# Kernel tuning notes

Hardware: AMD Instinct MI355X
Metric: run time of the kernel (lower is better)

The kernel has to match this reference:

```python
import jax, jax.numpy as jnp
import numpy as np

B, C, H, W = 8, 256, 64, 64
NH, FF, L, K = 8, 1024, 3, 64
THR = 0.5
DH = C // NH
SCALE = 1.0 / float(np.sqrt(DH))
N = H * W


def setup_inputs() -> dict:
    key = jax.random.key(0)
    ks = jax.random.split(key, 16)
    s = 0.02
    rn = lambda k, shape: (jax.random.normal(k, shape, jnp.float32) * s)
    return {
        "x": jax.random.normal(ks[0], (B, C, H, W), jnp.float32),
        "y": jax.random.normal(ks[1], (B, C, H, W), jnp.float32),
        "proj_w": rn(ks[2], (C, 2 * C)), "proj_b": rn(ks[3], (C,)),
        "sal_w": rn(ks[4], (1, C)), "sal_b": rn(ks[5], (1,)),
        "soft_w": rn(ks[6], (2, K, C)), "soft_b": rn(ks[7], (2, K)),
        "attn_in_w": rn(ks[8], (2, L, 3 * C, C)), "attn_in_b": rn(ks[9], (2, L, 3 * C)),
        "attn_out_w": rn(ks[10], (2, L, C, C)), "attn_out_b": rn(ks[11], (2, L, C)),
        "n1_g": jnp.ones((2, L, C), jnp.float32), "n1_b": jnp.zeros((2, L, C), jnp.float32),
        "ffn_w1": rn(ks[12], (2, L, FF, C)), "ffn_b1": rn(ks[13], (2, L, FF)),
        "ffn_w2": rn(ks[14], (2, L, C, FF)), "ffn_b2": rn(ks[15], (2, L, C)),
        "n2_g": jnp.ones((2, L, C), jnp.float32), "n2_b": jnp.zeros((2, L, C), jnp.float32),
    }


def _ln(t, g, b, eps=1e-5):
    m = t.mean(-1, keepdims=True)
    v = ((t - m) ** 2).mean(-1, keepdims=True)
    return (t - m) / jnp.sqrt(v + eps) * g + b


def _layers(q, kv, p, side):
    # q: [B,N,C] pixel queries, kv: [B,K,C] soft-pooled tokens
    for l in range(L):
        iw, ib = p["attn_in_w"][side, l], p["attn_in_b"][side, l]
        qq = (q @ iw[:C].T + ib[:C]).reshape(B, -1, NH, DH)
        kk = (kv @ iw[C:2 * C].T + ib[C:2 * C]).reshape(B, K, NH, DH)
        vv = (kv @ iw[2 * C:].T + ib[2 * C:]).reshape(B, K, NH, DH)
        att = jax.nn.softmax(jnp.einsum('bnhd,bkhd->bhnk', qq, kk) * SCALE, axis=-1)
        o = jnp.einsum('bhnk,bkhd->bnhd', att, vv).reshape(B, -1, C)
        o = o @ p["attn_out_w"][side, l].T + p["attn_out_b"][side, l]
        q = _ln(q + o, p["n1_g"][side, l], p["n1_b"][side, l])
        h = jax.nn.relu(q @ p["ffn_w1"][side, l].T + p["ffn_b1"][side, l])
        h = h @ p["ffn_w2"][side, l].T + p["ffn_b2"][side, l]
        q = _ln(q + h, p["n2_g"][side, l], p["n2_b"][side, l])
    return q


def _forward(x, y, proj_w, proj_b, sal_w, sal_b, soft_w, soft_b,
             attn_in_w, attn_in_b, attn_out_w, attn_out_b, n1_g, n1_b,
             ffn_w1, ffn_b1, ffn_w2, ffn_b2, n2_g, n2_b):
    p = dict(attn_in_w=attn_in_w, attn_in_b=attn_in_b, attn_out_w=attn_out_w,
             attn_out_b=attn_out_b, n1_g=n1_g, n1_b=n1_b, ffn_w1=ffn_w1,
             ffn_b1=ffn_b1, ffn_w2=ffn_w2, ffn_b2=ffn_b2, n2_g=n2_g, n2_b=n2_b)
    xc = jnp.concatenate([x, y], axis=1)                                  # [B,2C,H,W]
    feat = jnp.einsum('oc,bchw->bohw', proj_w, xc) + proj_b[None, :, None, None]
    sal = jnp.einsum('oc,bchw->bohw', sal_w, feat) + sal_b[None, :, None, None]  # [B,1,H,W]
    heat = jax.nn.sigmoid(sal)
    fg_mask = (heat >= THR).reshape(B, 1, N)
    bg_mask = (heat < 1.0 - THR).reshape(B, 1, N)
    fmap = feat.reshape(B, C, N)
    q0 = fmap.transpose(0, 2, 1)                                          # [B,N,C]
    out = fmap
    for side, hm in ((0, heat), (1, 1.0 - heat)):
        wf = feat * hm                                                    # [B,C,H,W]
        sw = (jnp.einsum('kc,bchw->bkhw', soft_w[side], wf)
              + soft_b[side][None, :, None, None]).reshape(B, K, N)       # [B,K,N]
        pool = jnp.einsum('bkn,bcn->bkc', sw, wf.reshape(B, C, N))        # [B,K,C]
        qs = _layers(q0, pool, p, side)                                   # [B,N,C]
        mask = fg_mask if side == 0 else bg_mask
        out = jnp.where(mask, qs.transpose(0, 2, 1), out)
    # per-image skip: if no fg or no bg pixels, keep original feature
    valid = fg_mask.any(axis=(1, 2)) & bg_mask.any(axis=(1, 2))           # [B]
    out = jnp.where(valid[:, None, None], out, fmap)
    return out.reshape(B, C, H, W)


def reference(x, y, proj_w, proj_b, sal_w, sal_b, soft_w, soft_b,
              attn_in_w, attn_in_b, attn_out_w, attn_out_b, n1_g, n1_b,
              ffn_w1, ffn_b1, ffn_w2, ffn_b2, n2_g, n2_b):
    return _forward(x, y, proj_w, proj_b, sal_w, sal_b, soft_w, soft_b,
                    attn_in_w, attn_in_b, attn_out_w, attn_out_b, n1_g, n1_b,
                    ffn_w1, ffn_b1, ffn_w2, ffn_b2, n2_g, n2_b)
```

## Files before the change

### kernel.cpp

```cpp
#include <hip/hip_runtime.h>
#include <stdint.h>

#define B_ 8
#define C_ 256
#define N_ 4096
#define K_ 64
#define NH_ 8
#define FF_ 1024
#define L_ 3
#define M_ (B_*N_)
#define SCALE_ 0.17677669529663687f

typedef float f32x4 __attribute__((ext_vector_type(4)));
typedef __bf16 v8bf __attribute__((ext_vector_type(8)));

__device__ __forceinline__ float b2f(unsigned short h){
  union { uint32_t u; float f; } v; v.u = ((uint32_t)h) << 16; return v.f;
}
__device__ __forceinline__ unsigned short f2b(float f){
  union { float f; uint32_t u; } v; v.f = f;
  uint32_t r = v.u + 0x7fffu + ((v.u >> 16) & 1u);
  return (unsigned short)(r >> 16);
}
__device__ __forceinline__ void gload_lds16(const void* g, void* l){
  __builtin_amdgcn_global_load_lds(
      (const __attribute__((address_space(1))) unsigned int*)g,
      (__attribute__((address_space(3))) unsigned int*)l, 16, 0, 0);
}

__global__ __launch_bounds__(256) void k_f32_to_bf16(const float* __restrict__ src,
                                                     unsigned short* __restrict__ dst, int n){
  int i4 = (blockIdx.x*256 + threadIdx.x)*4;
  if (i4 >= n) return;
  float4 v = *(const float4*)(src + i4);
  uint32_t p0 = (uint32_t)f2b(v.x) | ((uint32_t)f2b(v.y) << 16);
  uint32_t p1 = (uint32_t)f2b(v.z) | ((uint32_t)f2b(v.w) << 16);
  *(uint2*)(dst + i4) = make_uint2(p0, p1);
}

__global__ __launch_bounds__(256) void k_build_xcT(const float* __restrict__ x,
                                                   const float* __restrict__ y,
                                                   unsigned short* __restrict__ xcT){
  __shared__ float t[32][33];
  int b = blockIdx.z;
  int n0 = blockIdx.x*32, c0 = blockIdx.y*32;
  int tx = threadIdx.x, ty = threadIdx.y;
  const float* src = (c0 < 256) ? (x + ((size_t)b*256 + c0)*N_)
                                : (y + ((size_t)b*256 + (c0-256))*N_);
  #pragma unroll
  for (int i = 0; i < 4; i++){
    int cl = ty*4 + i;
    t[cl][tx] = src[(size_t)cl*N_ + n0 + tx];
  }
  __syncthreads();
  #pragma unroll
  for (int i = 0; i < 4; i++){
    int nl = ty*4 + i;
    xcT[((size_t)b*N_ + n0 + nl)*512 + c0 + tx] = f2b(t[tx][nl]);
  }
}

__global__ __launch_bounds__(256) void k_featmir(const float* __restrict__ featT,
                                                 unsigned short* __restrict__ featbf,
                                                 unsigned short* __restrict__ featC){
  __shared__ float t[32][33];
  int b = blockIdx.z;
  int n0 = blockIdx.x*32, c0 = blockIdx.y*32;
  int tx = threadIdx.x, ty = threadIdx.y;
  #pragma unroll
  for (int i = 0; i < 4; i++){
    int nl = ty*4 + i;
    size_t m = (size_t)b*N_ + n0 + nl;
    float v = featT[m*256 + c0 + tx];
    t[nl][tx] = v;
    featbf[m*256 + c0 + tx] = f2b(v);
  }
  __syncthreads();
  #pragma unroll
  for (int i = 0; i < 4; i++){
    int cl = ty*4 + i;
    featC[((size_t)b*256 + c0 + cl)*(size_t)N_ + n0 + tx] = f2b(t[tx][cl]);
  }
}

__global__ __launch_bounds__(512) void k_compute_u(const float* __restrict__ sal_w,
                                                   const float* __restrict__ proj_w,
                                                   const float* __restrict__ proj_b,
                                                   const float* __restrict__ sal_b,
                                                   double* __restrict__ u){
  int c2 = threadIdx.x;
  double acc = 0.0;
  for (int c = 0; c < 256; ++c)
    acc += (double)sal_w[c] * (double)proj_w[(size_t)c*512 + c2];
  u[c2] = acc;
  if (c2 == 0){
    double s0 = (double)sal_b[0];
    for (int c = 0; c < 256; ++c) s0 += (double)sal_w[c] * (double)proj_b[c];
    u[512] = s0;
  }
}

__global__ __launch_bounds__(256) void k_sal_part(const float* __restrict__ x,
                                                  const float* __restrict__ y,
                                                  const double* __restrict__ u,
                                                  double* __restrict__ part){
  int pix = blockIdx.x*256 + threadIdx.x;
  int cc = blockIdx.y;
  int b = pix >> 12, n = pix & 4095;
  int c0 = cc*32;
  const float* src = (c0 < 256) ? (x + ((size_t)b*256 + c0)*N_ + n)
                                : (y + ((size_t)b*256 + (c0-256))*N_ + n);
  const double* uu = u + c0;
  double acc = 0.0;
  #pragma unroll 8
  for (int c = 0; c < 32; ++c) acc += uu[c] * (double)src[(size_t)c*N_];
  part[(size_t)cc*32768 + pix] = acc;
}

__global__ __launch_bounds__(256) void k_sal_red(const double* __restrict__ part,
                                                 const double* __restrict__ u,
                                                 float* __restrict__ heat,
                                                 int* __restrict__ counts){
  int pix = blockIdx.x*256 + threadIdx.x;
  int b = pix >> 12;
  double acc = u[512];
  #pragma unroll
  for (int cc = 0; cc < 16; cc++) acc += part[(size_t)cc*32768 + pix];
  float hf = (float)(1.0 / (1.0 + exp(-acc)));
  heat[pix] = hf;
  unsigned long long mfg = __ballot(hf >= 0.5f);
  unsigned long long mbg = __ballot(hf < 0.5f);
  if ((threadIdx.x & 63) == 0){
    atomicAdd(&counts[b*2+0], (int)__popcll(mfg));
    atomicAdd(&counts[b*2+1], (int)__popcll(mbg));
  }
}

template<int EPI>
__global__ __launch_bounds__(256) void k_gemm_bt(
    const unsigned short* __restrict__ A, const unsigned short* __restrict__ W,
    const float* __restrict__ bias, void* __restrict__ out,
    int M, int N, int K){
  __shared__ unsigned short smem[2][2][128*64];
  int tid = threadIdx.x;
  int w = tid >> 6, l = tid & 63;
  int m0 = blockIdx.x * 128, n0 = blockIdx.y * 128;
  int wr = w >> 1, wc = w & 1;
  int lr = l & 15, lk = l >> 4;
  f32x4 acc[4][4] = {};
  int nt = K >> 6;
  #pragma unroll
  for (int i = 0; i < 4; i++){
    int idx = i*256 + tid;
    int row = idx >> 3, su = ((idx & 7) ^ (row & 7))*8;
    gload_lds16(A + (size_t)(m0+row)*K + su, &smem[0][0][idx*8]);
    gload_lds16(W + (size_t)(n0+row)*K + su, &smem[0][1][idx*8]);
  }
  __syncthreads();
  for (int t = 0; t < nt; ++t){
    int cur = t & 1;
    if (t + 1 < nt){
      int k0 = (t + 1) << 6;
      #pragma unroll
      for (int i = 0; i < 4; i++){
        int idx = i*256 + tid;
        int row = idx >> 3, su = ((idx & 7) ^ (row & 7))*8;
        gload_lds16(A + (size_t)(m0+row)*K + k0 + su, &smem[cur^1][0][idx*8]);
        gload_lds16(W + (size_t)(n0+row)*K + k0 + su, &smem[cur^1][1][idx*8]);
      }
    }
    const unsigned short* ldsA = smem[cur][0];
    const unsigned short* ldsB = smem[cur][1];
    #pragma unroll
    for (int kk = 0; kk < 2; kk++){
      v8bf af[4], bfr[4];
      #pragma unroll
      for (int f = 0; f < 4; f++){
        int ra = wr*64 + f*16 + lr;
        int rb2 = wc*64 + f*16 + lr;
        int u = kk*4 + lk;
        af[f]  = *(const v8bf*)(&ldsA[ra*64 + ((u ^ (ra&7))<<3)]);
        bfr[f] = *(const v8bf*)(&ldsB[rb2*64 + ((u ^ (rb2&7))<<3)]);
      }
      #pragma unroll
      for (int fi = 0; fi < 4; fi++)
        #pragma unroll
        for (int fj = 0; fj < 4; fj++)
          acc[fi][fj] = __builtin_amdgcn_mfma_f32_16x16x32_bf16(af[fi], bfr[fj], acc[fi][fj], 0, 0, 0);
    }
    __syncthreads();
  }
  if (EPI == 1 || EPI == 2){
    unsigned short* st = &smem[0][0][0];
    #pragma unroll
    for (int fj = 0; fj < 4; fj++){
      int col = wc*64 + fj*16 + lr;
      float bv = bias[n0 + col];
      #pragma unroll
      for (int fi = 0; fi < 4; fi++){
        int rl = wr*64 + fi*16 + lk*4;
        #pragma unroll
        for (int r = 0; r < 4; r++){
          float v = acc[fi][fj][r] + bv;
          if (EPI == 1) v = fmaxf(v, 0.f);
          st[(rl + r)*136 + col] = f2b(v);
        }
      }
    }
    __syncthreads();
    #pragma unroll
    for (int it = 0; it < 8; it++){
      int idx = it*256 + tid;
      int row = idx >> 4, c8 = (idx & 15)*8;
      *(uint4*)((unsigned short*)out + (size_t)(m0+row)*N + n0 + c8)
          = *(const uint4*)&st[row*136 + c8];
    }
  } else {
    #pragma unroll
    for (int fj = 0; fj < 4; fj++){
      int col = n0 + wc*64 + fj*16 + lr;
      float bv = bias[col];
      #pragma unroll
      for (int fi = 0; fi < 4; fi++){
        int rb = m0 + wr*64 + fi*16 + lk*4;
        #pragma unroll
        for (int r = 0; r < 4; r++){
          float v = acc[fi][fj][r] + bv;
          if (EPI == 3){
            int row = rb + r;
            ((unsigned short*)out)[((size_t)(row>>6)*256 + col)*64 + (row&63)] = f2b(v);
          } else {
            ((float*)out)[(size_t)(rb + r)*N + col] = v;
          }
        }
      }
    }
  }
}

__global__ __launch_bounds__(512) void k_ffn(
    const unsigned short* __restrict__ qb, const unsigned short* __restrict__ W1g,
    const float* __restrict__ b1g, const unsigned short* __restrict__ W2g,
    const float* __restrict__ b2g, unsigned short* __restrict__ outb){
  __shared__ unsigned short smem[73728];
  unsigned short* sA  = smem;
  unsigned short* sW1 = smem + 32768;
  unsigned short* sW2 = smem + 49152;
  unsigned short* sH  = smem + 65536;
  int tid = threadIdx.x;
  int w = tid >> 6, l = tid & 63;
  int m0 = blockIdx.x * 128;
  int wm = w >> 2;
  int wf = w & 3;
  int lr = l & 15, lk = l >> 4;

  #pragma unroll
  for (int i = 0; i < 8; i++){
    int idx = i*512 + tid;
    int row = idx >> 5, g = idx & 31;
    int su = (g & 24) | ((g & 7) ^ (row & 7));
    gload_lds16(qb + (size_t)(m0+row)*256 + su*8, &sA[idx*8]);
  }
  #pragma unroll
  for (int i = 0; i < 4; i++){
    int idx = i*512 + tid;
    int row = idx >> 5, g = idx & 31;
    int su = (g & 24) | ((g & 7) ^ (row & 7));
    gload_lds16(W1g + (size_t)row*256 + su*8, &sW1[idx*8]);
  }
  #pragma unroll
  for (int i = 0; i < 4; i++){
    int idx = i*512 + tid;
    int row = idx >> 3, g = idx & 7;
    int su = g ^ (row & 7);
    gload_lds16(W2g + (size_t)row*1024 + su*8, &sW2[idx*8]);
  }
  __syncthreads();

  f32x4 acc[4][4] = {};
  for (int cc = 0; cc < 16; ++cc){
    f32x4 hacc[4] = {};
    #pragma unroll
    for (int ks = 0; ks < 8; ks++){
      int g = ks*4 + lk;
      int rf = wf*16 + lr;
      v8bf bf1 = *(const v8bf*)&sW1[rf*256 + (((g & 24) | ((g & 7) ^ (rf & 7)))<<3)];
      #pragma unroll
      for (int f = 0; f < 4; f++){
        int ra = wm*64 + f*16 + lr;
        v8bf af = *(const v8bf*)&sA[ra*256 + (((g & 24) | ((g & 7) ^ (ra & 7)))<<3)];
        hacc[f] = __builtin_amdgcn_mfma_f32_16x16x32_bf16(af, bf1, hacc[f], 0, 0, 0);
      }
    }
    {
      int fc = wf*16 + lr;
      float b1v = b1g[cc*64 + fc];
      #pragma unroll
      for (int fi = 0; fi < 4; fi++){
        int mr0 = wm*64 + fi*16 + lk*4;
        #pragma unroll
        for (int r = 0; r < 4; r++){
          float v = fmaxf(hacc[fi][r] + b1v, 0.f);
          int mr = mr0 + r;
          sH[mr*64 + (((fc >> 3) ^ (mr & 7))<<3) + (fc & 7)] = f2b(v);
        }
      }
    }
    __syncthreads();
    if (cc + 1 < 16){
      int f0n = (cc+1)*64;
      #pragma unroll
      for (int i = 0; i < 4; i++){
        int idx = i*512 + tid;
        int row = idx >> 5, g = idx & 31;
        int su = (g & 24) | ((g & 7) ^ (row & 7));
        gload_lds16(W1g + (size_t)(f0n+row)*256 + su*8, &sW1[idx*8]);
      }
    }
    #pragma unroll
    for (int ks2 = 0; ks2 < 2; ks2++){
      int g = ks2*4 + lk;
      v8bf ha[4], wb[4];
      #pragma unroll
      for (int f = 0; f < 4; f++){
        int rh = wm*64 + f*16 + lr;
        ha[f] = *(const v8bf*)&sH[rh*64 + ((g ^ (rh & 7))<<3)];
      }
      #pragma unroll
      for (int f = 0; f < 4; f++){
        int rc = wf*64 + f*16 + lr;
        wb[f] = *(const v8bf*)&sW2[rc*64 + ((g ^ (rc & 7))<<3)];
      }
      #pragma unroll
      for (int fi = 0; fi < 4; fi++)
        #pragma unroll
        for (int fc = 0; fc < 4; fc++)
          acc[fi][fc] = __builtin_amdgcn_mfma_f32_16x16x32_bf16(ha[fi], wb[fc], acc[fi][fc], 0, 0, 0);
    }
    __syncthreads();
    if (cc + 1 < 16){
      int f0n = (cc+1)*64;
      #pragma unroll
      for (int i = 0; i < 4; i++){
        int idx = i*512 + tid;
        int row = idx >> 3, g = idx & 7;
        int su = g ^ (row & 7);
        gload_lds16(W2g + (size_t)row*1024 + f0n + su*8, &sW2[idx*8]);
      }
    }
  }
  unsigned short* st = smem;
  #pragma unroll
  for (int fc = 0; fc < 4; fc++){
    int col = wf*64 + fc*16 + lr;
    float bv = b2g[col];
    #pragma unroll
    for (int fi = 0; fi < 4; fi++){
      int rl = wm*64 + fi*16 + lk*4;
      #pragma unroll
      for (int r = 0; r < 4; r++)
        st[(rl + r)*264 + col] = f2b(acc[fi][fc][r] + bv);
    }
  }
  __syncthreads();
  #pragma unroll
  for (int it = 0; it < 8; it++){
    int idx = it*512 + tid;
    int row = idx >> 5, c8 = (idx & 31)*8;
    *(uint4*)(outb + (size_t)(m0+row)*256 + c8) = *(const uint4*)&st[row*264 + c8];
  }
}

__global__ __launch_bounds__(256) void k_swh(const float* __restrict__ g_all,
                                             const float* __restrict__ heat,
                                             const float* __restrict__ soft_b,
                                             unsigned short* __restrict__ swh){
  __shared__ float gl[64*129];
  __shared__ float hml[64];
  int tid = threadIdx.x;
  int blk = blockIdx.x;
  size_t m0 = (size_t)blk*64;
  int b = (int)(m0 >> 12), n0 = (int)(m0 & 4095);
  #pragma unroll
  for (int i = 0; i < 32; i++){
    int idx = i*256 + tid;
    int row = idx >> 7, col = idx & 127;
    gl[row*129 + col] = g_all[(m0 + row)*128 + col];
  }
  if (tid < 64) hml[tid] = heat[(size_t)b*4096 + n0 + tid];
  __syncthreads();
  int k = tid >> 2, j0 = (tid & 3)*16;
  #pragma unroll
  for (int s = 0; s < 2; s++){
    float sb = soft_b[s*64 + k];
    unsigned short vals[16];
    #pragma unroll
    for (int j = 0; j < 16; j++){
      int n = j0 + j;
      float h = hml[n];
      float hm = s ? (1.0f - h) : h;
      vals[j] = f2b((gl[n*129 + s*64 + k]*hm + sb)*hm);
    }
    unsigned short* dst = swh + (((size_t)b*2 + s)*64 + k)*4096 + n0 + j0;
    uint4 o0, o1;
    o0.x = vals[0] | ((uint32_t)vals[1]<<16);  o0.y = vals[2] | ((uint32_t)vals[3]<<16);
    o0.z = vals[4] | ((uint32_t)vals[5]<<16);  o0.w = vals[6] | ((uint32_t)vals[7]<<16);
    o1.x = vals[8] | ((uint32_t)vals[9]<<16);  o1.y = vals[10]| ((uint32_t)vals[11]<<16);
    o1.z = vals[12]| ((uint32_t)vals[13]<<16); o1.w = vals[14]| ((uint32_t)vals[15]<<16);
    *(uint4*)dst = o0;
    *(uint4*)(dst + 8) = o1;
  }
}

__global__ __launch_bounds__(256) void k_poolgemm(
    const unsigned short* __restrict__ swh, const unsigned short* __restrict__ featC,
    float* __restrict__ pp){
  __shared__ unsigned short ldsA[128*64];
  __shared__ unsigned short ldsB[128*64];
  int tid = threadIdx.x;
  int w = tid >> 6, l = tid & 63;
  int kc = blockIdx.x, nt = blockIdx.y, b = blockIdx.z;
  int wr = w >> 1, wc = w & 1;
  int lr = l & 15, lk = l >> 4;
  const unsigned short* A = swh  + (size_t)b*128*4096 + kc*512;
  const unsigned short* W = featC + ((size_t)b*256 + nt*128)*4096 + kc*512;
  f32x4 acc[4][4] = {};
  for (int k0 = 0; k0 < 512; k0 += 64){
    #pragma unroll
    for (int i = 0; i < 4; i++){
      int idx = i*256 + tid;
      int row = idx >> 3, su = (idx & 7) ^ (row & 7);
      gload_lds16(A + (size_t)row*4096 + k0 + su*8, &ldsA[idx*8]);
    }
    #pragma unroll
    for (int i = 0; i < 4; i++){
      int idx = i*256 + tid;
      int row = idx >> 3, su = (idx & 7) ^ (row & 7);
      gload_lds16(W + (size_t)row*4096 + k0 + su*8, &ldsB[idx*8]);
    }
    __syncthreads();
    #pragma unroll
    for (int kk = 0; kk < 2; kk++){
      v8bf af[4], bfr[4];
      #pragma unroll
      for (int f = 0; f < 4; f++){
        int ra = wr*64 + f*16 + lr;
        int rb2 = wc*64 + f*16 + lr;
        int u = kk*4 + lk;
        af[f]  = *(const v8bf*)(&ldsA[ra*64 + ((u ^ (ra&7))<<3)]);
        bfr[f] = *(const v8bf*)(&ldsB[rb2*64 + ((u ^ (rb2&7))<<3)]);
      }
      #pragma unroll
      for (int fi = 0; fi < 4; fi++)
        #pragma unroll
        for (int fj = 0; fj < 4; fj++)
          acc[fi][fj] = __builtin_amdgcn_mfma_f32_16x16x32_bf16(af[fi], bfr[fj], acc[fi][fj], 0, 0, 0);
    }
    __syncthreads();
  }
  float* dst = pp + ((size_t)kc*8 + b)*128*256;
  #pragma unroll
  for (int fj = 0; fj < 4; fj++){
    int col = nt*128 + wc*64 + fj*16 + lr;
    #pragma unroll
    for (int fi = 0; fi < 4; fi++){
      int rb = wr*64 + fi*16 + lk*4;
      #pragma unroll
      for (int r = 0; r < 4; r++)
        dst[(size_t)(rb + r)*256 + col] = acc[fi][fj][r];
    }
  }
}

__global__ __launch_bounds__(256) void k_pool2b(const float* __restrict__ pp,
                                                unsigned short* __restrict__ pool_bf_s){
  int bk = blockIdx.x, side = blockIdx.y, c = threadIdx.x;
  int b = bk >> 6, k = bk & 63;
  float s = 0.f;
  #pragma unroll
  for (int kc = 0; kc < 8; kc++)
    s += pp[(((size_t)kc*8 + b)*128 + side*64 + k)*256 + c];
  pool_bf_s[((size_t)side*512 + bk)*256 + c] = f2b(s);
}

__global__ __launch_bounds__(256) void k_attn2(
    const unsigned short* __restrict__ qq, const unsigned short* __restrict__ kk,
    const unsigned short* __restrict__ vvT, unsigned short* __restrict__ obf){
  __shared__ unsigned short sk[64*256];
  __shared__ unsigned short svT[256*64];
  __shared__ unsigned short sp[4][16*64];
  __shared__ unsigned short sow[4][16*32];
  int tid = threadIdx.x, w = tid >> 6, l = tid & 63;
  int blk = blockIdx.x, b = blk >> 6;
  int l15 = l & 15, lg = l >> 4;
  const uint4* ksrc = (const uint4*)(kk + (size_t)b*64*256);
  #pragma unroll
  for (int i = 0; i < 8; i++){
    int u = i*256 + tid;
    int row = u >> 5, j = u & 31;
    *(uint4*)&sk[row*256 + ((j ^ (row&7))<<3)] = ksrc[u];
  }
  const uint4* vsrc = (const uint4*)(vvT + (size_t)b*256*64);
  #pragma unroll
  for (int i = 0; i < 8; i++){
    int u = i*256 + tid;
    int row = u >> 3, j = u & 7;
    *(uint4*)&svT[row*64 + ((j ^ (row&7))<<3)] = vsrc[u];
  }
  __syncthreads();
  size_t qrow = (size_t)blk*64 + w*16 + l15;
  for (int h = 0; h < 8; h++){
    v8bf aq = *(const v8bf*)(qq + qrow*256 + h*32 + lg*8);
    f32x4 s[4];
    #pragma unroll
    for (int kt = 0; kt < 4; kt++){
      int row = kt*16 + l15;
      v8bf bk = *(const v8bf*)&sk[row*256 + (((h*4 + lg) ^ (row&7))<<3)];
      f32x4 z = {};
      s[kt] = __builtin_amdgcn_mfma_f32_16x16x32_bf16(aq, bk, z, 0, 0, 0);
    }
    #pragma unroll
    for (int r = 0; r < 4; r++){
      float v0 = s[0][r]*SCALE_, v1 = s[1][r]*SCALE_;
      float v2 = s[2][r]*SCALE_, v3 = s[3][r]*SCALE_;
      float mx = fmaxf(fmaxf(v0, v1), fmaxf(v2, v3));
      mx = fmaxf(mx, __shfl_xor(mx, 1));
      mx = fmaxf(mx, __shfl_xor(mx, 2));
      mx = fmaxf(mx, __shfl_xor(mx, 4));
      mx = fmaxf(mx, __shfl_xor(mx, 8));
      float e0 = __expf(v0-mx), e1 = __expf(v1-mx);
      float e2 = __expf(v2-mx), e3 = __expf(v3-mx);
      float sum = e0+e1+e2+e3;
      sum += __shfl_xor(sum, 1); sum += __shfl_xor(sum, 2);
      sum += __shfl_xor(sum, 4); sum += __shfl_xor(sum, 8);
      float inv = 1.0f/sum;
      s[0][r] = e0*inv; s[1][r] = e1*inv; s[2][r] = e2*inv; s[3][r] = e3*inv;
    }
    #pragma unroll
    for (int kt = 0; kt < 4; kt++){
      int colu = kt*2 + (l15>>3);
      #pragma unroll
      for (int r = 0; r < 4; r++){
        int row = lg*4 + r;
        sp[w][row*64 + ((colu ^ (row&7))<<3) + (l&7)] = f2b(s[kt][r]);
      }
    }
    f32x4 o[2] = {};
    #pragma unroll
    for (int k2 = 0; k2 < 2; k2++){
      v8bf pa = *(const v8bf*)&sp[w][l15*64 + (((k2*4 + lg) ^ (l15&7))<<3)];
      #pragma unroll
      for (int dt = 0; dt < 2; dt++){
        int vrow = h*32 + dt*16 + l15;
        v8bf bv = *(const v8bf*)&svT[vrow*64 + (((k2*4 + lg) ^ (vrow&7))<<3)];
        o[dt] = __builtin_amdgcn_mfma_f32_16x16x32_bf16(pa, bv, o[dt], 0, 0, 0);
      }
    }
    #pragma unroll
    for (int dt = 0; dt < 2; dt++)
      #pragma unroll
      for (int r = 0; r < 4; r++)
        sow[w][(lg*4 + r)*32 + dt*16 + l15] = f2b(o[dt][r]);
    uint4 ov = *(const uint4*)&sow[w][l15*32 + lg*8];
    *(uint4*)(obf + qrow*256 + h*32 + lg*8) = ov;
  }
}

template<int RF32>
__global__ __launch_bounds__(256) void k_ln2(
    const void* __restrict__ resid, const unsigned short* __restrict__ delta,
    const float* __restrict__ g, const float* __restrict__ bta,
    unsigned short* __restrict__ qout){
  int wv = threadIdx.x >> 6, l = threadIdx.x & 63;
  size_t m = (size_t)blockIdx.x*4 + wv;
  uint2 dv = *(const uint2*)(delta + m*256 + l*4);
  float d0 = b2f((unsigned short)(dv.x & 0xffff)), d1 = b2f((unsigned short)(dv.x >> 16));
  float d2 = b2f((unsigned short)(dv.y & 0xffff)), d3 = b2f((unsigned short)(dv.y >> 16));
  float x0, x1, x2, x3;
  if (RF32){
    float4 rv = *(const float4*)((const float*)resid + m*256 + l*4);
    x0 = rv.x+d0; x1 = rv.y+d1; x2 = rv.z+d2; x3 = rv.w+d3;
  } else {
    uint2 rv = *(const uint2*)((const unsigned short*)resid + m*256 + l*4);
    x0 = b2f((unsigned short)(rv.x & 0xffff)) + d0;
    x1 = b2f((unsigned short)(rv.x >> 16)) + d1;
    x2 = b2f((unsigned short)(rv.y & 0xffff)) + d2;
    x3 = b2f((unsigned short)(rv.y >> 16)) + d3;
  }
  float s = x0+x1+x2+x3;
  float ss = x0*x0+x1*x1+x2*x2+x3*x3;
  #pragma unroll
  for (int off = 32; off; off >>= 1){
    s  += __shfl_xor(s, off);
    ss += __shfl_xor(ss, off);
  }
  float mean = s * (1.0f/256.0f);
  float var = ss * (1.0f/256.0f) - mean*mean;
  float rstd = 1.0f / sqrtf(var + 1e-5f);
  float4 gv = *(const float4*)(g + l*4);
  float4 bv = *(const float4*)(bta + l*4);
  float y0 = (x0-mean)*rstd*gv.x + bv.x;
  float y1 = (x1-mean)*rstd*gv.y + bv.y;
  float y2 = (x2-mean)*rstd*gv.z + bv.z;
  float y3 = (x3-mean)*rstd*gv.w + bv.w;
  uint32_t p0 = (uint32_t)f2b(y0) | ((uint32_t)f2b(y1)<<16);
  uint32_t p1 = (uint32_t)f2b(y2) | ((uint32_t)f2b(y3)<<16);
  *(uint2*)(qout + m*256 + l*4) = make_uint2(p0,p1);
}

__global__ __launch_bounds__(256) void k_select(
    const unsigned short* __restrict__ qA, const unsigned short* __restrict__ qB,
    const float* __restrict__ featT, const float* __restrict__ heat,
    const int* __restrict__ counts, float* __restrict__ out){
  __shared__ float t[32][33];
  int b = blockIdx.z;
  int n0 = blockIdx.x*32, c0 = blockIdx.y*32;
  int tx = threadIdx.x, ty = threadIdx.y;
  bool valid = (counts[b*2] > 0) && (counts[b*2+1] > 0);
  #pragma unroll
  for (int i = 0; i < 4; i++){
    int nl = ty*4+i;
    size_t m = (size_t)b*4096 + n0 + nl;
    float v;
    if (!valid) v = featT[m*256 + c0 + tx];
    else {
      bool fg = heat[(size_t)b*4096 + n0 + nl] >= 0.5f;
      v = fg ? b2f(qA[m*256 + c0 + tx]) : b2f(qB[m*256 + c0 + tx]);
    }
    t[nl][tx] = v;
  }
  __syncthreads();
  #pragma unroll
  for (int i = 0; i < 4; i++){
    int cl = ty*4+i;
    out[((size_t)b*256 + c0 + cl)*4096 + n0 + tx] = t[tx][cl];
  }
}

extern "C" void kernel_launch(void* const* d_in, const int* in_sizes, int n_in,
                              void* d_out, int out_size, void* d_ws, size_t ws_size,
                              hipStream_t stream){
  const float* x         = (const float*)d_in[0];
  const float* y         = (const float*)d_in[1];
  const float* proj_w    = (const float*)d_in[2];
  const float* proj_b    = (const float*)d_in[3];
  const float* sal_w     = (const float*)d_in[4];
  const float* sal_b     = (const float*)d_in[5];
  const float* soft_w    = (const float*)d_in[6];
  const float* soft_b    = (const float*)d_in[7];
  const float* attn_in_w = (const float*)d_in[8];
  const float* attn_in_b = (const float*)d_in[9];
  const float* attn_out_w= (const float*)d_in[10];
  const float* attn_out_b= (const float*)d_in[11];
  const float* n1_g      = (const float*)d_in[12];
  const float* n1_b      = (const float*)d_in[13];
  const float* ffn_w1    = (const float*)d_in[14];
  const float* ffn_b1    = (const float*)d_in[15];
  const float* ffn_w2    = (const float*)d_in[16];
  const float* ffn_b2    = (const float*)d_in[17];
  const float* n2_g      = (const float*)d_in[18];
  const float* n2_b      = (const float*)d_in[19];
  float* out = (float*)d_out;

  char* p = (char*)d_ws;
  auto alloc = [&](size_t bytes){ char* r = p; p += (bytes + 255) & ~(size_t)255; return r; };
  unsigned short* hbf   = (unsigned short*)alloc((size_t)M_*FF_*2);
  unsigned short* xcT   = hbf;
  unsigned short* qq_bf = hbf;
  float* featT = (float*)alloc((size_t)M_*C_*4);
  unsigned short* qAb = (unsigned short*)alloc((size_t)M_*C_*2);
  unsigned short* swh = qAb;
  unsigned short* qBb = (unsigned short*)alloc((size_t)M_*C_*2);
  unsigned short* obf = (unsigned short*)alloc((size_t)M_*C_*2);
  unsigned short* featC = obf;
  unsigned short* featbf = (unsigned short*)alloc((size_t)M_*C_*2);
  unsigned short* tmpb = (unsigned short*)alloc((size_t)M_*C_*2);
  float* g_all = (float*)tmpb;
  float* pp    = (float*)alloc((size_t)8*8*128*256*4);
  double* salp = (double*)pp;
  unsigned short* pool_bf_s = (unsigned short*)alloc((size_t)2*512*256*2);
  unsigned short* kk_bf = (unsigned short*)alloc((size_t)B_*K_*C_*2);
  unsigned short* vvT_bf= (unsigned short*)alloc((size_t)B_*C_*K_*2);
  float* heat = (float*)alloc((size_t)B_*N_*4);
  double* u   = (double*)alloc(513*8);
  int* counts = (int*)alloc(64);
  float* zbias = (float*)alloc(512);
  unsigned short* projw_bf = (unsigned short*)alloc((size_t)C_*512*2);
  unsigned short* aiw_bf = (unsigned short*)alloc((size_t)2*L_*768*C_*2);
  unsigned short* aow_bf = (unsigned short*)alloc((size_t)2*L_*C_*C_*2);
  unsigned short* f1w_bf = (unsigned short*)alloc((size_t)2*L_*FF_*C_*2);
  unsigned short* f2w_bf = (unsigned short*)alloc((size_t)2*L_*C_*FF_*2);
  unsigned short* sw2_bf = (unsigned short*)alloc((size_t)2*K_*C_*2);

  hipMemsetAsync(counts, 0, 64, stream);
  hipMemsetAsync(zbias, 0, 512, stream);
  k_compute_u<<<1, 512, 0, stream>>>(sal_w, proj_w, proj_b, sal_b, u);
  k_sal_part<<<dim3(128, 16), 256, 0, stream>>>(x, y, u, salp);
  k_sal_red<<<128, 256, 0, stream>>>(salp, u, heat, counts);

  auto conv = [&](const float* s, unsigned short* d, size_t n){
    k_f32_to_bf16<<<(unsigned)((n/4 + 255)/256), 256, 0, stream>>>(s, d, (int)n);
  };
  conv(proj_w,     projw_bf, (size_t)C_*512);
  conv(attn_in_w,  aiw_bf,   (size_t)2*L_*768*C_);
  conv(attn_out_w, aow_bf,   (size_t)2*L_*C_*C_);
  conv(ffn_w1,     f1w_bf,   (size_t)2*L_*FF_*C_);
  conv(ffn_w2,     f2w_bf,   (size_t)2*L_*C_*FF_);
  conv(soft_w,     sw2_bf,   (size_t)2*K_*C_);

  k_build_xcT<<<dim3(N_/32, 512/32, B_), dim3(32,8), 0, stream>>>(x, y, xcT);
  k_gemm_bt<0><<<dim3(M_/128, C_/128), 256, 0, stream>>>(xcT, projw_bf, proj_b, featT, M_, C_, 512);
  k_featmir<<<dim3(N_/32, C_/32, B_), dim3(32,8), 0, stream>>>(featT, featbf, featC);

  k_gemm_bt<0><<<dim3(M_/128, 1), 256, 0, stream>>>(featbf, sw2_bf, zbias, g_all, M_, 128, C_);
  k_swh<<<M_/64, 256, 0, stream>>>(g_all, heat, soft_b, swh);
  k_poolgemm<<<dim3(8, 2, B_), 256, 0, stream>>>(swh, featC, pp);
  k_pool2b<<<dim3(512, 2), 256, 0, stream>>>(pp, pool_bf_s);

  for (int side = 0; side < 2; ++side){
    unsigned short* qb = side ? qBb : qAb;
    const unsigned short* poolS = pool_bf_s + (size_t)side*512*256;
    for (int lyr = 0; lyr < L_; ++lyr){
      int sl = side*L_ + lyr;
      const unsigned short* iw = aiw_bf + (size_t)sl*768*C_;
      const float* ib = attn_in_b + (size_t)sl*768;
      const unsigned short* qin = (lyr == 0) ? featbf : qb;
      k_gemm_bt<2><<<dim3(M_/128, C_/128), 256, 0, stream>>>(qin, iw, ib, qq_bf, M_, C_, C_);
      k_gemm_bt<2><<<dim3((B_*K_)/128, C_/128), 256, 0, stream>>>(poolS, iw + 256*C_, ib + 256, kk_bf, B_*K_, C_, C_);
      k_gemm_bt<3><<<dim3((B_*K_)/128, C_/128), 256, 0, stream>>>(poolS, iw + 512*C_, ib + 512, vvT_bf, B_*K_, C_, C_);
      k_attn2<<<M_/64, 256, 0, stream>>>(qq_bf, kk_bf, vvT_bf, obf);
      k_gemm_bt<2><<<dim3(M_/128, C_/128), 256, 0, stream>>>(obf, aow_bf + (size_t)sl*C_*C_, attn_out_b + (size_t)sl*C_, tmpb, M_, C_, C_);
      if (lyr == 0)
        k_ln2<1><<<M_/4, 256, 0, stream>>>(featT, tmpb, n1_g + (size_t)sl*C_, n1_b + (size_t)sl*C_, qb);
      else
        k_ln2<0><<<M_/4, 256, 0, stream>>>(qb, tmpb, n1_g + (size_t)sl*C_, n1_b + (size_t)sl*C_, qb);
      k_ffn<<<M_/128, 512, 0, stream>>>(qb, f1w_bf + (size_t)sl*FF_*C_, ffn_b1 + (size_t)sl*FF_,
                                        f2w_bf + (size_t)sl*C_*FF_, ffn_b2 + (size_t)sl*C_, tmpb);
      k_ln2<0><<<M_/4, 256, 0, stream>>>(qb, tmpb, n2_g + (size_t)sl*C_, n2_b + (size_t)sl*C_, qb);
    }
  }
  k_select<<<dim3(N_/32, C_/32, B_), dim3(32,8), 0, stream>>>(qAb, qBb, featT, heat, counts, out);
}
```

Baseline: 855.4 us.

## Fuse residual+LayerNorm into FFN epilogue, merge K/V projections, reswizzle hidden LDS

The FFN kernel now adds the residual read from its LDS copy of the input rows, computes the per-row LayerNorm with shuffle and LDS reductions, and writes the normalized result straight to q. This removes a separate k_ln2 launch and a round trip of the tmp buffer per layer. The K and V projections are combined into one k_kv launch that selects the weight slice by blockIdx.z. The sH swizzle key also mixes in higher row bits to cut LDS bank conflicts. The variance is now computed in one pass as E[x^2]-mean^2, and the fused epilogue adds reductions and syncs at the end of the FFN kernel.

New measurement: 822.6 us. -3.8%, faster.

```diff
diff --git a/kernel.cpp b/kernel.cpp
--- a/kernel.cpp
+++ b/kernel.cpp
@@ -238,10 +238,86 @@
   }
 }
 
+__global__ __launch_bounds__(256) void k_kv(
+    const unsigned short* __restrict__ pool, const unsigned short* __restrict__ iw,
+    const float* __restrict__ ib, unsigned short* __restrict__ kk_bf,
+    unsigned short* __restrict__ vvT_bf){
+  __shared__ unsigned short smem[2][2][128*64];
+  int tid = threadIdx.x;
+  int w = tid >> 6, l = tid & 63;
+  int m0 = blockIdx.x * 128, n0 = blockIdx.y * 128;
+  int isv = blockIdx.z;
+  const unsigned short* W = iw + (size_t)(isv ? 512 : 256)*256;
+  const float* bias = ib + (isv ? 512 : 256);
+  int wr = w >> 1, wc = w & 1;
+  int lr = l & 15, lk = l >> 4;
+  f32x4 acc[4][4] = {};
+  #pragma unroll
+  for (int i = 0; i < 4; i++){
+    int idx = i*256 + tid;
+    int row = idx >> 3, su = ((idx & 7) ^ (row & 7))*8;
+    gload_lds16(pool + (size_t)(m0+row)*256 + su, &smem[0][0][idx*8]);
+    gload_lds16(W + (size_t)(n0+row)*256 + su, &smem[0][1][idx*8]);
+  }
+  __syncthreads();
+  for (int t = 0; t < 4; ++t){
+    int cur = t & 1;
+    if (t + 1 < 4){
+      int k0 = (t + 1) << 6;
+      #pragma unroll
+      for (int i = 0; i < 4; i++){
+        int idx = i*256 + tid;
+        int row = idx >> 3, su = ((idx & 7) ^ (row & 7))*8;
+        gload_lds16(pool + (size_t)(m0+row)*256 + k0 + su, &smem[cur^1][0][idx*8]);
+        gload_lds16(W + (size_t)(n0+row)*256 + k0 + su, &smem[cur^1][1][idx*8]);
+      }
+    }
+    const unsigned short* ldsA = smem[cur][0];
+    const unsigned short* ldsB = smem[cur][1];
+    #pragma unroll
+    for (int kk = 0; kk < 2; kk++){
+      v8bf af[4], bfr[4];
+      #pragma unroll
+      for (int f = 0; f < 4; f++){
+        int ra = wr*64 + f*16 + lr;
+        int rb2 = wc*64 + f*16 + lr;
+        int u = kk*4 + lk;
+        af[f]  = *(const v8bf*)(&ldsA[ra*64 + ((u ^ (ra&7))<<3)]);
+        bfr[f] = *(const v8bf*)(&ldsB[rb2*64 + ((u ^ (rb2&7))<<3)]);
+      }
+      #pragma unroll
+      for (int fi = 0; fi < 4; fi++)
+        #pragma unroll
+        for (int fj = 0; fj < 4; fj++)
+          acc[fi][fj] = __builtin_amdgcn_mfma_f32_16x16x32_bf16(af[fi], bfr[fj], acc[fi][fj], 0, 0, 0);
+    }
+    __syncthreads();
+  }
+  #pragma unroll
+  for (int fj = 0; fj < 4; fj++){
+    int col = n0 + wc*64 + fj*16 + lr;
+    float bv = bias[col];
+    #pragma unroll
+    for (int fi = 0; fi < 4; fi++){
+      int rb = m0 + wr*64 + fi*16 + lk*4;
+      #pragma unroll
+      for (int r = 0; r < 4; r++){
+        float v = acc[fi][fj][r] + bv;
+        int row = rb + r;
+        if (isv)
+          vvT_bf[((size_t)(row>>6)*256 + col)*64 + (row&63)] = f2b(v);
+        else
+          kk_bf[(size_t)row*256 + col] = f2b(v);
+      }
+    }
+  }
+}
+
 __global__ __launch_bounds__(512) void k_ffn(
     const unsigned short* __restrict__ qb, const unsigned short* __restrict__ W1g,
     const float* __restrict__ b1g, const unsigned short* __restrict__ W2g,
-    const float* __restrict__ b2g, unsigned short* __restrict__ outb){
+    const float* __restrict__ b2g, const float* __restrict__ n2g,
+    const float* __restrict__ n2b, unsigned short* __restrict__ qout){
   __shared__ unsigned short smem[73728];
   unsigned short* sA  = smem;
   unsigned short* sW1 = smem + 32768;
@@ -302,7 +378,8 @@
         for (int r = 0; r < 4; r++){
           float v = fmaxf(hacc[fi][r] + b1v, 0.f);
           int mr = mr0 + r;
-          sH[mr*64 + (((fc >> 3) ^ (mr & 7))<<3) + (fc & 7)] = f2b(v);
+          int key = (mr ^ (mr >> 3)) & 7;
+          sH[mr*64 + (((fc >> 3) ^ key)<<3) + (fc & 7)] = f2b(v);
         }
       }
     }
@@ -324,7 +401,8 @@
       #pragma unroll
       for (int f = 0; f < 4; f++){
         int rh = wm*64 + f*16 + lr;
-        ha[f] = *(const v8bf*)&sH[rh*64 + ((g ^ (rh & 7))<<3)];
+        int key = (rh ^ (rh >> 3)) & 7;
+        ha[f] = *(const v8bf*)&sH[rh*64 + ((g ^ key)<<3)];
       }
       #pragma unroll
       for (int f = 0; f < 4; f++){
@@ -349,17 +427,73 @@
       }
     }
   }
-  unsigned short* st = smem;
+
+  float b2v[4], gv[4], bev[4];
   #pragma unroll
   for (int fc = 0; fc < 4; fc++){
     int col = wf*64 + fc*16 + lr;
-    float bv = b2g[col];
-    #pragma unroll
-    for (int fi = 0; fi < 4; fi++){
-      int rl = wm*64 + fi*16 + lk*4;
-      #pragma unroll
-      for (int r = 0; r < 4; r++)
-        st[(rl + r)*264 + col] = f2b(acc[fi][fc][r] + bv);
+    b2v[fc] = b2g[col];
+    gv[fc]  = n2g[col];
+    bev[fc] = n2b[col];
+  }
+  #pragma unroll
+  for (int fi = 0; fi < 4; fi++){
+    #pragma unroll
+    for (int r = 0; r < 4; r++){
+      int row = wm*64 + fi*16 + lk*4 + r;
+      #pragma unroll
+      for (int fc = 0; fc < 4; fc++){
+        int col = wf*64 + fc*16 + lr;
+        int cu2 = col >> 3;
+        int su = (cu2 & 24) | ((cu2 & 7) ^ (row & 7));
+        float resid = b2f(sA[row*256 + su*8 + (col & 7)]);
+        acc[fi][fc][r] += b2v[fc] + resid;
+      }
+    }
+  }
+  float* psum = (float*)(smem + 32768);
+  float* psq  = psum + 512;
+  float* mstd = psq + 512;
+  #pragma unroll
+  for (int fi = 0; fi < 4; fi++){
+    #pragma unroll
+    for (int r = 0; r < 4; r++){
+      float s = acc[fi][0][r] + acc[fi][1][r] + acc[fi][2][r] + acc[fi][3][r];
+      float q = acc[fi][0][r]*acc[fi][0][r] + acc[fi][1][r]*acc[fi][1][r]
+              + acc[fi][2][r]*acc[fi][2][r] + acc[fi][3][r]*acc[fi][3][r];
+      s += __shfl_xor(s, 1); s += __shfl_xor(s, 2);
+      s += __shfl_xor(s, 4); s += __shfl_xor(s, 8);
+      q += __shfl_xor(q, 1); q += __shfl_xor(q, 2);
+      q += __shfl_xor(q, 4); q += __shfl_xor(q, 8);
+      if (lr == 0){
+        int row = wm*64 + fi*16 + lk*4 + r;
+        psum[row*4 + wf] = s;
+        psq[row*4 + wf]  = q;
+      }
+    }
+  }
+  __syncthreads();
+  if (tid < 128){
+    float s = psum[tid*4] + psum[tid*4+1] + psum[tid*4+2] + psum[tid*4+3];
+    float q = psq[tid*4] + psq[tid*4+1] + psq[tid*4+2] + psq[tid*4+3];
+    float mean = s * (1.0f/256.0f);
+    float var = q * (1.0f/256.0f) - mean*mean;
+    mstd[tid*2]   = mean;
+    mstd[tid*2+1] = 1.0f / sqrtf(var + 1e-5f);
+  }
+  __syncthreads();
+  unsigned short* st = smem;
+  #pragma unroll
+  for (int fi = 0; fi < 4; fi++){
+    #pragma unroll
+    for (int r = 0; r < 4; r++){
+      int rowl = wm*64 + fi*16 + lk*4 + r;
+      float mean = mstd[rowl*2], rstd = mstd[rowl*2+1];
+      #pragma unroll
+      for (int fc = 0; fc < 4; fc++){
+        int col = wf*64 + fc*16 + lr;
+        st[rowl*264 + col] = f2b((acc[fi][fc][r] - mean)*rstd*gv[fc] + bev[fc]);
+      }
     }
   }
   __syncthreads();
@@ -367,7 +501,7 @@
   for (int it = 0; it < 8; it++){
     int idx = it*512 + tid;
     int row = idx >> 5, c8 = (idx & 31)*8;
-    *(uint4*)(outb + (size_t)(m0+row)*256 + c8) = *(const uint4*)&st[row*264 + c8];
+    *(uint4*)(qout + (size_t)(m0+row)*256 + c8) = *(const uint4*)&st[row*264 + c8];
   }
 }
 
@@ -726,8 +860,7 @@
       const float* ib = attn_in_b + (size_t)sl*768;
       const unsigned short* qin = (lyr == 0) ? featbf : qb;
       k_gemm_bt<2><<<dim3(M_/128, C_/128), 256, 0, stream>>>(qin, iw, ib, qq_bf, M_, C_, C_);
-      k_gemm_bt<2><<<dim3((B_*K_)/128, C_/128), 256, 0, stream>>>(poolS, iw + 256*C_, ib + 256, kk_bf, B_*K_, C_, C_);
-      k_gemm_bt<3><<<dim3((B_*K_)/128, C_/128), 256, 0, stream>>>(poolS, iw + 512*C_, ib + 512, vvT_bf, B_*K_, C_, C_);
+      k_kv<<<dim3(4, 2, 2), 256, 0, stream>>>(poolS, iw, ib, kk_bf, vvT_bf);
       k_attn2<<<M_/64, 256, 0, stream>>>(qq_bf, kk_bf, vvT_bf, obf);
       k_gemm_bt<2><<<dim3(M_/128, C_/128), 256, 0, stream>>>(obf, aow_bf + (size_t)sl*C_*C_, attn_out_b + (size_t)sl*C_, tmpb, M_, C_, C_);
       if (lyr == 0)
@@ -735,8 +868,8 @@
       else
         k_ln2<0><<<M_/4, 256, 0, stream>>>(qb, tmpb, n1_g + (size_t)sl*C_, n1_b + (size_t)sl*C_, qb);
       k_ffn<<<M_/128, 512, 0, stream>>>(qb, f1w_bf + (size_t)sl*FF_*C_, ffn_b1 + (size_t)sl*FF_,
-                                        f2w_bf + (size_t)sl*C_*FF_, ffn_b2 + (size_t)sl*C_, tmpb);
-      k_ln2<0><<<M_/4, 256, 0, stream>>>(qb, tmpb, n2_g + (size_t)sl*C_, n2_b + (size_t)sl*C_, qb);
+                                        f2w_bf + (size_t)sl*C_*FF_, ffn_b2 + (size_t)sl*C_,
+                                        n2_g + (size_t)sl*C_, n2_b + (size_t)sl*C_, qb);
     }
   }
   k_select<<<dim3(N_/32, C_/32, B_), dim3(32,8), 0, stream>>>(qAb, qBb, featT, heat, counts, out);
```

## Retile fused FFN to 64-row blocks and merge K/V projection launches

Applied to the files above, without the earlier changes.

The fused FFN kernel moves from 128-row tiles with 512 threads and 64-wide hidden chunks to 64-row tiles with 256 threads and 32-wide hidden chunks, using a new LDS swizzle for the narrower H and W2 tiles. LDS per block drops from about 144KB to about 68KB, and the grid doubles to 512 blocks, aiming for more resident blocks per CU and better CU coverage. The cost is twice as many weight reloads per output row, and a per-warp accumulator of 2x8 tiles instead of 4x4. Separately, the K and V projection GEMMs are merged into one kernel launch that picks the weight slice via blockIdx.z, removing one launch per layer.

Result: slower. 924.9 us (+8.1%).

```diff
diff --git a/kernel.cpp b/kernel.cpp
--- a/kernel.cpp
+++ b/kernel.cpp
@@ -238,125 +238,200 @@
   }
 }
 
-__global__ __launch_bounds__(512) void k_ffn(
+__global__ __launch_bounds__(256) void k_kv(
+    const unsigned short* __restrict__ pool, const unsigned short* __restrict__ iw,
+    const float* __restrict__ ib, unsigned short* __restrict__ kk_bf,
+    unsigned short* __restrict__ vvT_bf){
+  __shared__ unsigned short smem[2][2][128*64];
+  int tid = threadIdx.x;
+  int w = tid >> 6, l = tid & 63;
+  int m0 = blockIdx.x * 128, n0 = blockIdx.y * 128;
+  int isv = blockIdx.z;
+  const unsigned short* W = iw + (size_t)(isv ? 512 : 256)*256;
+  const float* bias = ib + (isv ? 512 : 256);
+  int wr = w >> 1, wc = w & 1;
+  int lr = l & 15, lk = l >> 4;
+  f32x4 acc[4][4] = {};
+  #pragma unroll
+  for (int i = 0; i < 4; i++){
+    int idx = i*256 + tid;
+    int row = idx >> 3, su = ((idx & 7) ^ (row & 7))*8;
+    gload_lds16(pool + (size_t)(m0+row)*256 + su, &smem[0][0][idx*8]);
+    gload_lds16(W + (size_t)(n0+row)*256 + su, &smem[0][1][idx*8]);
+  }
+  __syncthreads();
+  for (int t = 0; t < 4; ++t){
+    int cur = t & 1;
+    if (t + 1 < 4){
+      int k0 = (t + 1) << 6;
+      #pragma unroll
+      for (int i = 0; i < 4; i++){
+        int idx = i*256 + tid;
+        int row = idx >> 3, su = ((idx & 7) ^ (row & 7))*8;
+        gload_lds16(pool + (size_t)(m0+row)*256 + k0 + su, &smem[cur^1][0][idx*8]);
+        gload_lds16(W + (size_t)(n0+row)*256 + k0 + su, &smem[cur^1][1][idx*8]);
+      }
+    }
+    const unsigned short* ldsA = smem[cur][0];
+    const unsigned short* ldsB = smem[cur][1];
+    #pragma unroll
+    for (int kk = 0; kk < 2; kk++){
+      v8bf af[4], bfr[4];
+      #pragma unroll
+      for (int f = 0; f < 4; f++){
+        int ra = wr*64 + f*16 + lr;
+        int rb2 = wc*64 + f*16 + lr;
+        int u = kk*4 + lk;
+        af[f]  = *(const v8bf*)(&ldsA[ra*64 + ((u ^ (ra&7))<<3)]);
+        bfr[f] = *(const v8bf*)(&ldsB[rb2*64 + ((u ^ (rb2&7))<<3)]);
+      }
+      #pragma unroll
+      for (int fi = 0; fi < 4; fi++)
+        #pragma unroll
+        for (int fj = 0; fj < 4; fj++)
+          acc[fi][fj] = __builtin_amdgcn_mfma_f32_16x16x32_bf16(af[fi], bfr[fj], acc[fi][fj], 0, 0, 0);
+    }
+    __syncthreads();
+  }
+  #pragma unroll
+  for (int fj = 0; fj < 4; fj++){
+    int col = n0 + wc*64 + fj*16 + lr;
+    float bv = bias[col];
+    #pragma unroll
+    for (int fi = 0; fi < 4; fi++){
+      int rb = m0 + wr*64 + fi*16 + lk*4;
+      #pragma unroll
+      for (int r = 0; r < 4; r++){
+        float v = acc[fi][fj][r] + bv;
+        int row = rb + r;
+        if (isv)
+          vvT_bf[((size_t)(row>>6)*256 + col)*64 + (row&63)] = f2b(v);
+        else
+          kk_bf[(size_t)row*256 + col] = f2b(v);
+      }
+    }
+  }
+}
+
+__global__ __launch_bounds__(256) void k_ffn64(
     const unsigned short* __restrict__ qb, const unsigned short* __restrict__ W1g,
     const float* __restrict__ b1g, const unsigned short* __restrict__ W2g,
     const float* __restrict__ b2g, unsigned short* __restrict__ outb){
-  __shared__ unsigned short smem[73728];
+  __shared__ unsigned short smem[34816];
   unsigned short* sA  = smem;
-  unsigned short* sW1 = smem + 32768;
-  unsigned short* sW2 = smem + 49152;
-  unsigned short* sH  = smem + 65536;
+  unsigned short* sW1 = smem + 16384;
+  unsigned short* sW2 = smem + 24576;
+  unsigned short* sH  = smem + 32768;
   int tid = threadIdx.x;
   int w = tid >> 6, l = tid & 63;
-  int m0 = blockIdx.x * 128;
-  int wm = w >> 2;
-  int wf = w & 3;
+  int m0 = blockIdx.x * 64;
+  int wm = w >> 1, wf = w & 1;
   int lr = l & 15, lk = l >> 4;
 
   #pragma unroll
   for (int i = 0; i < 8; i++){
-    int idx = i*512 + tid;
+    int idx = i*256 + tid;
     int row = idx >> 5, g = idx & 31;
     int su = (g & 24) | ((g & 7) ^ (row & 7));
     gload_lds16(qb + (size_t)(m0+row)*256 + su*8, &sA[idx*8]);
   }
   #pragma unroll
   for (int i = 0; i < 4; i++){
-    int idx = i*512 + tid;
+    int idx = i*256 + tid;
     int row = idx >> 5, g = idx & 31;
     int su = (g & 24) | ((g & 7) ^ (row & 7));
     gload_lds16(W1g + (size_t)row*256 + su*8, &sW1[idx*8]);
   }
   #pragma unroll
   for (int i = 0; i < 4; i++){
-    int idx = i*512 + tid;
-    int row = idx >> 3, g = idx & 7;
-    int su = g ^ (row & 7);
+    int idx = i*256 + tid;
+    int row = idx >> 2, g = idx & 3;
+    int su = g ^ (((row >> 2) ^ row) & 3);
     gload_lds16(W2g + (size_t)row*1024 + su*8, &sW2[idx*8]);
   }
   __syncthreads();
 
-  f32x4 acc[4][4] = {};
-  for (int cc = 0; cc < 16; ++cc){
-    f32x4 hacc[4] = {};
+  f32x4 acc[2][8] = {};
+  for (int cc = 0; cc < 32; ++cc){
+    f32x4 hacc[2] = {};
     #pragma unroll
     for (int ks = 0; ks < 8; ks++){
       int g = ks*4 + lk;
       int rf = wf*16 + lr;
       v8bf bf1 = *(const v8bf*)&sW1[rf*256 + (((g & 24) | ((g & 7) ^ (rf & 7)))<<3)];
       #pragma unroll
-      for (int f = 0; f < 4; f++){
-        int ra = wm*64 + f*16 + lr;
+      for (int f = 0; f < 2; f++){
+        int ra = wm*32 + f*16 + lr;
         v8bf af = *(const v8bf*)&sA[ra*256 + (((g & 24) | ((g & 7) ^ (ra & 7)))<<3)];
         hacc[f] = __builtin_amdgcn_mfma_f32_16x16x32_bf16(af, bf1, hacc[f], 0, 0, 0);
       }
     }
     {
       int fc = wf*16 + lr;
-      float b1v = b1g[cc*64 + fc];
-      #pragma unroll
-      for (int fi = 0; fi < 4; fi++){
-        int mr0 = wm*64 + fi*16 + lk*4;
+      float b1v = b1g[cc*32 + fc];
+      #pragma unroll
+      for (int fi = 0; fi < 2; fi++){
+        int mr0 = wm*32 + fi*16 + lk*4;
         #pragma unroll
         for (int r = 0; r < 4; r++){
           float v = fmaxf(hacc[fi][r] + b1v, 0.f);
           int mr = mr0 + r;
-          sH[mr*64 + (((fc >> 3) ^ (mr & 7))<<3) + (fc & 7)] = f2b(v);
+          int key = ((mr >> 2) ^ mr) & 3;
+          sH[mr*32 + (((fc >> 3) ^ key)<<3) + (fc & 7)] = f2b(v);
         }
       }
     }
     __syncthreads();
-    if (cc + 1 < 16){
-      int f0n = (cc+1)*64;
+    if (cc + 1 < 32){
+      int f0n = (cc+1)*32;
       #pragma unroll
       for (int i = 0; i < 4; i++){
-        int idx = i*512 + tid;
+        int idx = i*256 + tid;
         int row = idx >> 5, g = idx & 31;
         int su = (g & 24) | ((g & 7) ^ (row & 7));
         gload_lds16(W1g + (size_t)(f0n+row)*256 + su*8, &sW1[idx*8]);
       }
     }
-    #pragma unroll
-    for (int ks2 = 0; ks2 < 2; ks2++){
-      int g = ks2*4 + lk;
-      v8bf ha[4], wb[4];
-      #pragma unroll
-      for (int f = 0; f < 4; f++){
-        int rh = wm*64 + f*16 + lr;
-        ha[f] = *(const v8bf*)&sH[rh*64 + ((g ^ (rh & 7))<<3)];
-      }
-      #pragma unroll
-      for (int f = 0; f < 4; f++){
-        int rc = wf*64 + f*16 + lr;
-        wb[f] = *(const v8bf*)&sW2[rc*64 + ((g ^ (rc & 7))<<3)];
-      }
-      #pragma unroll
-      for (int fi = 0; fi < 4; fi++)
+    {
+      v8bf ha[2], wb[8];
+      #pragma unroll
+      for (int f = 0; f < 2; f++){
+        int rh = wm*32 + f*16 + lr;
+        int key = ((rh >> 2) ^ rh) & 3;
+        ha[f] = *(const v8bf*)&sH[rh*32 + ((lk ^ key)<<3)];
+      }
+      #pragma unroll
+      for (int f = 0; f < 8; f++){
+        int rc = wf*128 + f*16 + lr;
+        int key = ((rc >> 2) ^ rc) & 3;
+        wb[f] = *(const v8bf*)&sW2[rc*32 + ((lk ^ key)<<3)];
+      }
+      #pragma unroll
+      for (int fi = 0; fi < 2; fi++)
         #pragma unroll
-        for (int fc = 0; fc < 4; fc++)
+        for (int fc = 0; fc < 8; fc++)
           acc[fi][fc] = __builtin_amdgcn_mfma_f32_16x16x32_bf16(ha[fi], wb[fc], acc[fi][fc], 0, 0, 0);
     }
     __syncthreads();
-    if (cc + 1 < 16){
-      int f0n = (cc+1)*64;
+    if (cc + 1 < 32){
+      int f0n = (cc+1)*32;
       #pragma unroll
       for (int i = 0; i < 4; i++){
-        int idx = i*512 + tid;
-        int row = idx >> 3, g = idx & 7;
-        int su = g ^ (row & 7);
+        int idx = i*256 + tid;
+        int row = idx >> 2, g = idx & 3;
+        int su = g ^ (((row >> 2) ^ row) & 3);
         gload_lds16(W2g + (size_t)row*1024 + f0n + su*8, &sW2[idx*8]);
       }
     }
   }
   unsigned short* st = smem;
   #pragma unroll
-  for (int fc = 0; fc < 4; fc++){
-    int col = wf*64 + fc*16 + lr;
+  for (int fc = 0; fc < 8; fc++){
+    int col = wf*128 + fc*16 + lr;
     float bv = b2g[col];
     #pragma unroll
-    for (int fi = 0; fi < 4; fi++){
-      int rl = wm*64 + fi*16 + lk*4;
+    for (int fi = 0; fi < 2; fi++){
+      int rl = wm*32 + fi*16 + lk*4;
       #pragma unroll
       for (int r = 0; r < 4; r++)
         st[(rl + r)*264 + col] = f2b(acc[fi][fc][r] + bv);
@@ -365,7 +440,7 @@
   __syncthreads();
   #pragma unroll
   for (int it = 0; it < 8; it++){
-    int idx = it*512 + tid;
+    int idx = it*256 + tid;
     int row = idx >> 5, c8 = (idx & 31)*8;
     *(uint4*)(outb + (size_t)(m0+row)*256 + c8) = *(const uint4*)&st[row*264 + c8];
   }
@@ -726,16 +801,15 @@
       const float* ib = attn_in_b + (size_t)sl*768;
       const unsigned short* qin = (lyr == 0) ? featbf : qb;
       k_gemm_bt<2><<<dim3(M_/128, C_/128), 256, 0, stream>>>(qin, iw, ib, qq_bf, M_, C_, C_);
-      k_gemm_bt<2><<<dim3((B_*K_)/128, C_/128), 256, 0, stream>>>(poolS, iw + 256*C_, ib + 256, kk_bf, B_*K_, C_, C_);
-      k_gemm_bt<3><<<dim3((B_*K_)/128, C_/128), 256, 0, stream>>>(poolS, iw + 512*C_, ib + 512, vvT_bf, B_*K_, C_, C_);
+      k_kv<<<dim3(4, 2, 2), 256, 0, stream>>>(poolS, iw, ib, kk_bf, vvT_bf);
       k_attn2<<<M_/64, 256, 0, stream>>>(qq_bf, kk_bf, vvT_bf, obf);
       k_gemm_bt<2><<<dim3(M_/128, C_/128), 256, 0, stream>>>(obf, aow_bf + (size_t)sl*C_*C_, attn_out_b + (size_t)sl*C_, tmpb, M_, C_, C_);
       if (lyr == 0)
         k_ln2<1><<<M_/4, 256, 0, stream>>>(featT, tmpb, n1_g + (size_t)sl*C_, n1_b + (size_t)sl*C_, qb);
       else
         k_ln2<0><<<M_/4, 256, 0, stream>>>(qb, tmpb, n1_g + (size_t)sl*C_, n1_b + (size_t)sl*C_, qb);
-      k_ffn<<<M_/128, 512, 0, stream>>>(qb, f1w_bf + (size_t)sl*FF_*C_, ffn_b1 + (size_t)sl*FF_,
-                                        f2w_bf + (size_t)sl*C_*FF_, ffn_b2 + (size_t)sl*C_, tmpb);
+      k_ffn64<<<M_/64, 256, 0, stream>>>(qb, f1w_bf + (size_t)sl*FF_*C_, ffn_b1 + (size_t)sl*FF_,
+                                         f2w_bf + (size_t)sl*C_*FF_, ffn_b2 + (size_t)sl*C_, tmpb);
       k_ln2<0><<<M_/4, 256, 0, stream>>>(qb, tmpb, n2_g + (size_t)sl*C_, n2_b + (size_t)sl*C_, qb);
     }
   }
```
